# Performance work log

Measured on AMD Instinct MI355X. Metric: run time of the kernel, lower is better.

Reference implementation:

```python
import jax, jax.numpy as jnp
import numpy as np

N_NODES = 100000
N_EDGES = 1600000
D_IN = 128
D_HID = 128


def gcn_layer(x, src, dst, ew, W, b, n):
    """PyG GCNConv with normalize=True, add_self_loops=True (self-loop weight 1)."""
    h = x @ W  # [n, d_out]
    # degree includes self-loop weight 1.0
    deg = jax.ops.segment_sum(ew, dst, num_segments=n) + 1.0  # [n]
    dis = jnp.where(deg > 0, jax.lax.rsqrt(deg), 0.0)  # deg^{-1/2}
    norm = dis[src] * ew * dis[dst]  # [E]
    agg = jax.ops.segment_sum(norm[:, None] * h[src], dst, num_segments=n)
    # self-loop term: norm_ii = dis[i] * 1.0 * dis[i]
    agg = agg + (dis * dis)[:, None] * h
    return agg + b


def prelu(x, alpha):
    return jnp.where(x >= 0, x, alpha * x)


def setup_inputs() -> dict:
    key = jax.random.key(0)
    ks = jax.random.split(key, 12)
    x = jax.random.normal(ks[0], (N_NODES, D_IN), dtype=jnp.float32)
    edge_index = jax.random.randint(ks[1], (2, N_EDGES), 0, N_NODES, dtype=jnp.int64)
    edge_weight = jax.random.uniform(ks[2], (N_EDGES,), dtype=jnp.float32)
    s1 = 1.0 / np.sqrt(D_IN)
    s2 = 1.0 / np.sqrt(D_HID)
    params = {
        "W1": jax.random.normal(ks[3], (D_IN, D_HID), dtype=jnp.float32) * s1,
        "b1": jnp.zeros((D_HID,), dtype=jnp.float32),
        "a1": jnp.full((D_HID,), 0.25, dtype=jnp.float32),
        "W2": jax.random.normal(ks[4], (D_HID, D_HID), dtype=jnp.float32) * s2,
        "b2": jnp.zeros((D_HID,), dtype=jnp.float32),
        "a2": jnp.full((D_HID,), 0.25, dtype=jnp.float32),
        "W3": jax.random.normal(ks[5], (D_HID, D_HID), dtype=jnp.float32) * s2,
        "b3": jnp.zeros((D_HID,), dtype=jnp.float32),
        "a3": jnp.full((D_HID,), 0.25, dtype=jnp.float32),
    }
    return {"x": x, "edge_index": edge_index, "edge_weight": edge_weight, **params}


def reference(x, edge_index, edge_weight, W1, b1, a1, W2, b2, a2, W3, b3, a3):
    src, dst = edge_index[0], edge_index[1]
    n = x.shape[0]
    h = prelu(gcn_layer(x, src, dst, edge_weight, W1, b1, n), a1)
    h = prelu(gcn_layer(h, src, dst, edge_weight, W2, b2, n), a2)
    h = prelu(gcn_layer(h, src, dst, edge_weight, W3, b3, n), a3)
    return h
```

## Files before the change

kernel.cpp:

```cpp
#include <hip/hip_runtime.h>

#define N_NODES 100000
#define N_EDGES 1600000
#define D 128
#define TILE_ROWS 32
#define CHUNK 4096
#define NC ((N_EDGES + CHUNK - 1) / CHUNK)
#define NB ((N_NODES + 255) / 256)
#define HLEN (NB * NC)
#define SCAN_BLK ((HLEN + 1023) / 1024)

typedef unsigned int uint;
typedef unsigned long long u64;
typedef short short8 __attribute__((ext_vector_type(8)));
typedef float f32x4 __attribute__((ext_vector_type(4)));

__device__ inline ushort f2bf(float f) {
    union { float f; uint u; } v; v.f = f;
    uint r = v.u + 0x7fffu + ((v.u >> 16) & 1u);
    return (ushort)(r >> 16);
}
__device__ inline float bf2f(ushort b) {
    union { uint u; float f; } v; v.u = ((uint)b) << 16;
    return v.f;
}


__global__ __launch_bounds__(256) void k_hist(const int* __restrict__ dst, int* __restrict__ H) {
    __shared__ int hist[NB];
    int c = blockIdx.x;
    for (int i = threadIdx.x; i < NB; i += 256) hist[i] = 0;
    __syncthreads();
    int base = c * CHUNK;
    int lim = N_EDGES - base; if (lim > CHUNK) lim = CHUNK;
    for (int k = threadIdx.x; k < lim; k += 256)
        atomicAdd(&hist[dst[base + k] >> 8], 1);
    __syncthreads();
    for (int i = threadIdx.x; i < NB; i += 256) H[c * NB + i] = hist[i];
}

__global__ __launch_bounds__(256) void k_scanA(const int* __restrict__ H, int* __restrict__ HOFF,
                                               int* __restrict__ bsum) {
    __shared__ int sd[256];
    int t = threadIdx.x;
    int base = blockIdx.x * 1024 + t * 4;
    int v[4];
#pragma unroll
    for (int j = 0; j < 4; ++j) {
        int l = base + j;
        v[j] = (l < HLEN) ? H[(l % NC) * NB + (l / NC)] : 0;
    }
    int lsum = v[0] + v[1] + v[2] + v[3];
    sd[t] = lsum;
    __syncthreads();
    for (int off = 1; off < 256; off <<= 1) {
        int x = (t >= off) ? sd[t - off] : 0;
        __syncthreads();
        sd[t] += x;
        __syncthreads();
    }
    int excl = sd[t] - lsum;
    if (base + 0 < HLEN) HOFF[base + 0] = excl;
    if (base + 1 < HLEN) HOFF[base + 1] = excl + v[0];
    if (base + 2 < HLEN) HOFF[base + 2] = excl + v[0] + v[1];
    if (base + 3 < HLEN) HOFF[base + 3] = excl + v[0] + v[1] + v[2];
    if (t == 255) bsum[blockIdx.x] = sd[255];
}

__global__ void k_scanB(int* __restrict__ bsum) {
    if (blockIdx.x == 0 && threadIdx.x == 0) {
        int total = 0;
        for (int b = 0; b < SCAN_BLK; ++b) { int x = bsum[b]; bsum[b] = total; total += x; }
    }
}

__global__ void k_scanC(int* __restrict__ HOFF, const int* __restrict__ bsum) {
    int i = blockIdx.x * blockDim.x + threadIdx.x;
    if (i < HLEN) HOFF[i] += bsum[i >> 10];
}

__global__ __launch_bounds__(256) void k_pscat(const int* __restrict__ src, const int* __restrict__ dst,
                                               const float* __restrict__ ew, const int* __restrict__ HOFF,
                                               u64* __restrict__ tmp) {
    __shared__ int cur[NB];
    int c = blockIdx.x;
    for (int i = threadIdx.x; i < NB; i += 256) cur[i] = HOFF[i * NC + c];
    __syncthreads();
    int base = c * CHUNK;
    int lim = N_EDGES - base; if (lim > CHUNK) lim = CHUNK;
    for (int k = threadIdx.x; k < lim; k += 256) {
        int e = base + k;
        int s = src[e], t = dst[e];
        u64 q = (u64)llrintf(ew[e] * 1073741824.0f);
        int pos = atomicAdd(&cur[t >> 8], 1);
        tmp[pos] = (u64)s | ((u64)t << 17) | (q << 34);
    }
}

__global__ __launch_bounds__(256) void k_b1(const int* __restrict__ HOFF, const u64* __restrict__ tmp,
                                            float* __restrict__ dis, int* __restrict__ rowptr) {
    __shared__ int cnt[256];
    __shared__ u64 degq[256];
    __shared__ int sd[256];
    __shared__ int sbeg, send;
    int b = blockIdx.x, t = threadIdx.x;
    cnt[t] = 0; degq[t] = 0;
    if (t == 0) {
        sbeg = HOFF[b * NC];
        send = (b + 1 < NB) ? HOFF[(b + 1) * NC] : N_EDGES;
    }
    __syncthreads();
    int beg = sbeg, end = send, lo = b << 8;
    for (int e = beg + t; e < end; e += 256) {
        u64 r = tmp[e];
        int loc = (int)((r >> 17) & 0x1FFFF) - lo;
        atomicAdd(&cnt[loc], 1);
        atomicAdd(&degq[loc], r >> 34);
    }
    __syncthreads();
    int n = lo + t;
    if (n < N_NODES) {
        float deg = (float)((double)degq[t] * (1.0 / 1073741824.0));
        dis[n] = rsqrtf(deg + 1.0f);
    }
    int v = cnt[t];
    sd[t] = v;
    __syncthreads();
    for (int off = 1; off < 256; off <<= 1) {
        int x = (t >= off) ? sd[t - off] : 0;
        __syncthreads();
        sd[t] += x;
        __syncthreads();
    }
    if (n < N_NODES) rowptr[n] = beg + sd[t] - v;
    if (b == NB - 1 && t == 0) rowptr[N_NODES] = N_EDGES;
}

__global__ __launch_bounds__(256) void k_b2(const int* __restrict__ HOFF, const u64* __restrict__ tmp,
                                            const float* __restrict__ dis, const int* __restrict__ rowptr,
                                            int2* __restrict__ edges) {
    __shared__ int cur[256];
    __shared__ float disl[256];
    __shared__ int sbeg, send;
    int b = blockIdx.x, t = threadIdx.x;
    int lo = b << 8;
    int n = lo + t;
    cur[t] = (n < N_NODES) ? rowptr[n] : 0;
    disl[t] = (n < N_NODES) ? dis[n] : 0.0f;
    if (t == 0) {
        sbeg = HOFF[b * NC];
        send = (b + 1 < NB) ? HOFF[(b + 1) * NC] : N_EDGES;
    }
    __syncthreads();
    for (int e = sbeg + t; e < send; e += 256) {
        u64 r = tmp[e];
        int s = (int)(r & 0x1FFFF);
        int loc = (int)((r >> 17) & 0x1FFFF) - lo;
        float w = (float)(r >> 34) * (1.0f / 1073741824.0f);
        float coef = dis[s] * w * disl[loc];
        int pos = atomicAdd(&cur[loc], 1);
        edges[pos] = make_int2(s, __float_as_int(coef));
    }
}

__global__ void k_wsplit(const float* __restrict__ W, ushort* __restrict__ Wht,
                         ushort* __restrict__ Wlt) {
    int i = blockIdx.x * 256 + threadIdx.x;
    int k = i >> 7, c = i & 127;
    float w = W[i];
    ushort wh = f2bf(w);
    ushort wl = f2bf(w - bf2f(wh));
    int j = k >> 3;
    int off = c * 128 + (((j ^ (c & 7)) << 3) | (k & 7));
    Wht[off] = wh;
    Wlt[off] = wl;
}

__global__ __launch_bounds__(256) void k_gemm_mfma(
    const float* __restrict__ x, const ushort* __restrict__ Wht,
    const ushort* __restrict__ Wlt, ushort* __restrict__ hb)
{
    __shared__ ushort WH[16384];
    __shared__ ushort WL[16384];
    __shared__ ushort XH[4096];
    __shared__ ushort XL[4096];

    const int tx = threadIdx.x;
    const int row0 = blockIdx.x * TILE_ROWS;

    for (int i = tx; i < 2048; i += 256) {
        ((uint4*)WH)[i] = ((const uint4*)Wht)[i];
        ((uint4*)WL)[i] = ((const uint4*)Wlt)[i];
    }

    {
        int m = tx * 2;
        int r = m >> 4;
        int jb = m & 15;
        const float* xp = x + (size_t)(row0 + r) * D;
#pragma unroll
        for (int c = 0; c < 2; ++c) {
            int j = jb + c;
            float4 a0 = *(const float4*)(xp + j * 8);
            float4 a1 = *(const float4*)(xp + j * 8 + 4);
            float v[8] = {a0.x, a0.y, a0.z, a0.w, a1.x, a1.y, a1.z, a1.w};
            uint4 uh, ul;
            uint* ph = (uint*)&uh; uint* pl = (uint*)&ul;
#pragma unroll
            for (int e = 0; e < 4; ++e) {
                ushort h0 = f2bf(v[2 * e]),     h1 = f2bf(v[2 * e + 1]);
                ushort l0 = f2bf(v[2 * e] - bf2f(h0));
                ushort l1 = f2bf(v[2 * e + 1] - bf2f(h1));
                ph[e] = (uint)h0 | ((uint)h1 << 16);
                pl[e] = (uint)l0 | ((uint)l1 << 16);
            }
            int off = r * 16 + (j ^ (r & 7));
            ((uint4*)XH)[off] = uh;
            ((uint4*)XL)[off] = ul;
        }
    }
    __syncthreads();

    const int wv = tx >> 6;
    const int lane = tx & 63;
    const int lr = lane & 15;
    const int g = lane >> 4;

    f32x4 acc[2][2] = {};

    const int c0 = wv * 32 + lr;
    const int c1 = c0 + 16;

#pragma unroll
    for (int ks = 0; ks < 4; ++ks) {
        int co = ((ks * 4 + g) ^ (lr & 7)) << 3;
        short8 ah0 = *(short8*)&XH[lr * 128 + co];
        short8 ah1 = *(short8*)&XH[(16 + lr) * 128 + co];
        short8 al0 = *(short8*)&XL[lr * 128 + co];
        short8 al1 = *(short8*)&XL[(16 + lr) * 128 + co];
        short8 bh0 = *(short8*)&WH[c0 * 128 + co];
        short8 bh1 = *(short8*)&WH[c1 * 128 + co];
        short8 bl0 = *(short8*)&WL[c0 * 128 + co];
        short8 bl1 = *(short8*)&WL[c1 * 128 + co];

        acc[0][0] = __builtin_amdgcn_mfma_f32_16x16x32_bf16(ah0, bh0, acc[0][0], 0, 0, 0);
        acc[0][1] = __builtin_amdgcn_mfma_f32_16x16x32_bf16(ah0, bh1, acc[0][1], 0, 0, 0);
        acc[1][0] = __builtin_amdgcn_mfma_f32_16x16x32_bf16(ah1, bh0, acc[1][0], 0, 0, 0);
        acc[1][1] = __builtin_amdgcn_mfma_f32_16x16x32_bf16(ah1, bh1, acc[1][1], 0, 0, 0);
        acc[0][0] = __builtin_amdgcn_mfma_f32_16x16x32_bf16(al0, bh0, acc[0][0], 0, 0, 0);
        acc[0][1] = __builtin_amdgcn_mfma_f32_16x16x32_bf16(al0, bh1, acc[0][1], 0, 0, 0);
        acc[1][0] = __builtin_amdgcn_mfma_f32_16x16x32_bf16(al1, bh0, acc[1][0], 0, 0, 0);
        acc[1][1] = __builtin_amdgcn_mfma_f32_16x16x32_bf16(al1, bh1, acc[1][1], 0, 0, 0);
        acc[0][0] = __builtin_amdgcn_mfma_f32_16x16x32_bf16(ah0, bl0, acc[0][0], 0, 0, 0);
        acc[0][1] = __builtin_amdgcn_mfma_f32_16x16x32_bf16(ah0, bl1, acc[0][1], 0, 0, 0);
        acc[1][0] = __builtin_amdgcn_mfma_f32_16x16x32_bf16(ah1, bl0, acc[1][0], 0, 0, 0);
        acc[1][1] = __builtin_amdgcn_mfma_f32_16x16x32_bf16(ah1, bl1, acc[1][1], 0, 0, 0);
    }

#pragma unroll
    for (int rt = 0; rt < 2; ++rt) {
#pragma unroll
        for (int ct = 0; ct < 2; ++ct) {
            int colb = wv * 32 + ct * 16 + lr;
#pragma unroll
            for (int e = 0; e < 4; ++e) {
                int row = row0 + rt * 16 + g * 4 + e;
                hb[(size_t)row * D + colb] = f2bf(acc[rt][ct][e]);
            }
        }
    }
}

__global__ __launch_bounds__(256) void k_gather(
    const int* __restrict__ rowptr, const int2* __restrict__ edges,
    const ushort* __restrict__ hb, const float* __restrict__ dis,
    const float* __restrict__ b, const float* __restrict__ alpha,
    float* __restrict__ out)
{
    int gid = blockIdx.x * 256 + threadIdx.x;
    int n = gid >> 6;
    if (n >= N_NODES) return;
    int lane = gid & 63;
    int q = lane >> 4;
    int c0 = (lane & 15) * 8;

    int beg = rowptr[n], end = rowptr[n + 1];
    float acc[8] = {0.f, 0.f, 0.f, 0.f, 0.f, 0.f, 0.f, 0.f};

    int e = beg + q;
    for (; e + 12 < end; e += 16) {
        int2 sc0 = edges[e];
        int2 sc1 = edges[e + 4];
        int2 sc2 = edges[e + 8];
        int2 sc3 = edges[e + 12];
        uint4 hv0 = *(const uint4*)&hb[(size_t)sc0.x * D + c0];
        uint4 hv1 = *(const uint4*)&hb[(size_t)sc1.x * D + c0];
        uint4 hv2 = *(const uint4*)&hb[(size_t)sc2.x * D + c0];
        uint4 hv3 = *(const uint4*)&hb[(size_t)sc3.x * D + c0];
        float ca = __int_as_float(sc0.y);
        float cb = __int_as_float(sc1.y);
        float cc = __int_as_float(sc2.y);
        float cd = __int_as_float(sc3.y);
#pragma unroll
        for (int j = 0; j < 4; ++j) {
            uint w0 = ((const uint*)&hv0)[j];
            uint w1 = ((const uint*)&hv1)[j];
            uint w2 = ((const uint*)&hv2)[j];
            uint w3 = ((const uint*)&hv3)[j];
            acc[2 * j]     = fmaf(ca, __uint_as_float(w0 << 16),         acc[2 * j]);
            acc[2 * j + 1] = fmaf(ca, __uint_as_float(w0 & 0xffff0000u), acc[2 * j + 1]);
            acc[2 * j]     = fmaf(cb, __uint_as_float(w1 << 16),         acc[2 * j]);
            acc[2 * j + 1] = fmaf(cb, __uint_as_float(w1 & 0xffff0000u), acc[2 * j + 1]);
            acc[2 * j]     = fmaf(cc, __uint_as_float(w2 << 16),         acc[2 * j]);
            acc[2 * j + 1] = fmaf(cc, __uint_as_float(w2 & 0xffff0000u), acc[2 * j + 1]);
            acc[2 * j]     = fmaf(cd, __uint_as_float(w3 << 16),         acc[2 * j]);
            acc[2 * j + 1] = fmaf(cd, __uint_as_float(w3 & 0xffff0000u), acc[2 * j + 1]);
        }
    }
    for (; e < end; e += 4) {
        int2 sc = edges[e];
        float c = __int_as_float(sc.y);
        uint4 hv = *(const uint4*)&hb[(size_t)sc.x * D + c0];
#pragma unroll
        for (int j = 0; j < 4; ++j) {
            uint w = ((const uint*)&hv)[j];
            acc[2 * j]     = fmaf(c, __uint_as_float(w << 16),         acc[2 * j]);
            acc[2 * j + 1] = fmaf(c, __uint_as_float(w & 0xffff0000u), acc[2 * j + 1]);
        }
    }

#pragma unroll
    for (int j = 0; j < 8; ++j) {
        acc[j] += __shfl_xor(acc[j], 16);
        acc[j] += __shfl_xor(acc[j], 32);
    }

    if (q == 0) {
        float di = dis[n];
        float d2 = di * di;
        uint4 hv = *(const uint4*)&hb[(size_t)n * D + c0];
        float r[8];
#pragma unroll
        for (int j = 0; j < 4; ++j) {
            uint w = ((const uint*)&hv)[j];
            float lo = __uint_as_float(w << 16);
            float hi = __uint_as_float(w & 0xffff0000u);
            r[2 * j]     = acc[2 * j]     + d2 * lo + b[c0 + 2 * j];
            r[2 * j + 1] = acc[2 * j + 1] + d2 * hi + b[c0 + 2 * j + 1];
        }
#pragma unroll
        for (int j = 0; j < 8; ++j) {
            float av = alpha[c0 + j];
            r[j] = r[j] >= 0.f ? r[j] : av * r[j];
        }
        *(float4*)&out[(size_t)n * D + c0]     = make_float4(r[0], r[1], r[2], r[3]);
        *(float4*)&out[(size_t)n * D + c0 + 4] = make_float4(r[4], r[5], r[6], r[7]);
    }
}


extern "C" void kernel_launch(void* const* d_in, const int* in_sizes, int n_in,
                              void* d_out, int out_size, void* d_ws, size_t ws_size,
                              hipStream_t stream) {
    const float* x   = (const float*)d_in[0];
    const int*   ei  = (const int*)d_in[1];
    const float* ew  = (const float*)d_in[2];
    const float* W1  = (const float*)d_in[3];
    const float* b1  = (const float*)d_in[4];
    const float* a1  = (const float*)d_in[5];
    const float* W2  = (const float*)d_in[6];
    const float* b2  = (const float*)d_in[7];
    const float* a2  = (const float*)d_in[8];
    const float* W3  = (const float*)d_in[9];
    const float* b3  = (const float*)d_in[10];
    const float* a3  = (const float*)d_in[11];

    const int* src = ei;
    const int* dst = ei + N_EDGES;

    float* out = (float*)d_out;

    ushort* hb    = (ushort*)d_ws;
    int2*   edges = (int2*)(hb + (size_t)N_NODES * D);
    u64*    tmp   = (u64*)(edges + N_EDGES);
    int*    H     = (int*)(tmp + N_EDGES);
    int*    HOFF  = H + HLEN;
    int*    bsum  = HOFF + HLEN;
    float*  dis   = (float*)(bsum + 256);
    int*    rowptr= (int*)(dis + N_NODES);
    ushort* wsp   = (ushort*)(rowptr + N_NODES + 2);
    ushort* Wht1 = wsp;              ushort* Wlt1 = wsp + 16384;
    ushort* Wht2 = wsp + 2 * 16384;  ushort* Wlt2 = wsp + 3 * 16384;
    ushort* Wht3 = wsp + 4 * 16384;  ushort* Wlt3 = wsp + 5 * 16384;

    k_wsplit<<<64, 256, 0, stream>>>(W1, Wht1, Wlt1);
    k_wsplit<<<64, 256, 0, stream>>>(W2, Wht2, Wlt2);
    k_wsplit<<<64, 256, 0, stream>>>(W3, Wht3, Wlt3);

    k_hist<<<NC, 256, 0, stream>>>(dst, H);
    k_scanA<<<SCAN_BLK, 256, 0, stream>>>(H, HOFF, bsum);
    k_scanB<<<1, 1, 0, stream>>>(bsum);
    k_scanC<<<(HLEN + 255) / 256, 256, 0, stream>>>(HOFF, bsum);
    k_pscat<<<NC, 256, 0, stream>>>(src, dst, ew, HOFF, tmp);
    k_b1<<<NB, 256, 0, stream>>>(HOFF, tmp, dis, rowptr);
    k_b2<<<NB, 256, 0, stream>>>(HOFF, tmp, dis, rowptr, edges);

    const int gemm_blocks   = N_NODES / TILE_ROWS;
    const int gather_blocks = (N_NODES * 64) / 256;

    k_gemm_mfma<<<gemm_blocks, 256, 0, stream>>>(x, Wht1, Wlt1, hb);
    k_gather<<<gather_blocks, 256, 0, stream>>>(rowptr, edges, hb, dis, b1, a1, out);
    k_gemm_mfma<<<gemm_blocks, 256, 0, stream>>>(out, Wht2, Wlt2, hb);
    k_gather<<<gather_blocks, 256, 0, stream>>>(rowptr, edges, hb, dis, b2, a2, out);
    k_gemm_mfma<<<gemm_blocks, 256, 0, stream>>>(out, Wht3, Wlt3, hb);
    k_gather<<<gather_blocks, 256, 0, stream>>>(rowptr, edges, hb, dis, b3, a3, out);
}
```

Baseline: 415.9 us.

## Persistent GEMM blocks, parallel block-sum scan, merged weight split, shallower gather unroll

The GEMM becomes a grid-stride persistent kernel with 512 blocks, so the 64 KB bf16 hi/lo weight tile is loaded into shared memory once per block rather than once per 32-row tile. The single-thread block-sum scan is replaced by a 256-thread shared-memory scan, and the three weight-split launches are merged into one. The gather inner loop is unrolled by 2 instead of 4 edges, which lowers register pressure and may raise occupancy but leaves fewer independent loads in flight. The persistent GEMM adds an extra barrier per tile and only 512 blocks may underfill the device.

After: 384.3 us. 1.08x faster.

```diff
diff --git a/kernel.cpp b/kernel.cpp
--- a/kernel.cpp
+++ b/kernel.cpp
@@ -4,6 +4,8 @@
 #define N_EDGES 1600000
 #define D 128
 #define TILE_ROWS 32
+#define N_TILES (N_NODES / TILE_ROWS)
+#define GEMM_BLOCKS 512
 #define CHUNK 4096
 #define NC ((N_EDGES + CHUNK - 1) / CHUNK)
 #define NB ((N_NODES + 255) / 256)
@@ -67,11 +69,19 @@
     if (t == 255) bsum[blockIdx.x] = sd[255];
 }
 
-__global__ void k_scanB(int* __restrict__ bsum) {
-    if (blockIdx.x == 0 && threadIdx.x == 0) {
-        int total = 0;
-        for (int b = 0; b < SCAN_BLK; ++b) { int x = bsum[b]; bsum[b] = total; total += x; }
-    }
+__global__ __launch_bounds__(256) void k_scanB(int* __restrict__ bsum) {
+    __shared__ int sd[256];
+    int t = threadIdx.x;
+    int v = (t < SCAN_BLK) ? bsum[t] : 0;
+    sd[t] = v;
+    __syncthreads();
+    for (int off = 1; off < 256; off <<= 1) {
+        int x = (t >= off) ? sd[t - off] : 0;
+        __syncthreads();
+        sd[t] += x;
+        __syncthreads();
+    }
+    if (t < SCAN_BLK) bsum[t] = sd[t] - v;
 }
 
 __global__ void k_scanC(int* __restrict__ HOFF, const int* __restrict__ bsum) {
@@ -163,9 +173,14 @@
     }
 }
 
-__global__ void k_wsplit(const float* __restrict__ W, ushort* __restrict__ Wht,
-                         ushort* __restrict__ Wlt) {
-    int i = blockIdx.x * 256 + threadIdx.x;
+__global__ void k_wsplit3(const float* __restrict__ W1, const float* __restrict__ W2,
+                          const float* __restrict__ W3, ushort* __restrict__ wsp) {
+    int gid = blockIdx.x * 256 + threadIdx.x;
+    int l = gid >> 14;
+    int i = gid & 16383;
+    const float* W = (l == 0) ? W1 : (l == 1) ? W2 : W3;
+    ushort* Wht = wsp + l * 32768;
+    ushort* Wlt = Wht + 16384;
     int k = i >> 7, c = i & 127;
     float w = W[i];
     ushort wh = f2bf(w);
@@ -186,86 +201,88 @@
     __shared__ ushort XL[4096];
 
     const int tx = threadIdx.x;
-    const int row0 = blockIdx.x * TILE_ROWS;
 
     for (int i = tx; i < 2048; i += 256) {
         ((uint4*)WH)[i] = ((const uint4*)Wht)[i];
         ((uint4*)WL)[i] = ((const uint4*)Wlt)[i];
     }
-
-    {
-        int m = tx * 2;
-        int r = m >> 4;
-        int jb = m & 15;
-        const float* xp = x + (size_t)(row0 + r) * D;
-#pragma unroll
-        for (int c = 0; c < 2; ++c) {
-            int j = jb + c;
-            float4 a0 = *(const float4*)(xp + j * 8);
-            float4 a1 = *(const float4*)(xp + j * 8 + 4);
-            float v[8] = {a0.x, a0.y, a0.z, a0.w, a1.x, a1.y, a1.z, a1.w};
-            uint4 uh, ul;
-            uint* ph = (uint*)&uh; uint* pl = (uint*)&ul;
-#pragma unroll
-            for (int e = 0; e < 4; ++e) {
-                ushort h0 = f2bf(v[2 * e]),     h1 = f2bf(v[2 * e + 1]);
-                ushort l0 = f2bf(v[2 * e] - bf2f(h0));
-                ushort l1 = f2bf(v[2 * e + 1] - bf2f(h1));
-                ph[e] = (uint)h0 | ((uint)h1 << 16);
-                pl[e] = (uint)l0 | ((uint)l1 << 16);
-            }
-            int off = r * 16 + (j ^ (r & 7));
-            ((uint4*)XH)[off] = uh;
-            ((uint4*)XL)[off] = ul;
-        }
-    }
-    __syncthreads();
 
     const int wv = tx >> 6;
     const int lane = tx & 63;
     const int lr = lane & 15;
     const int g = lane >> 4;
-
-    f32x4 acc[2][2] = {};
-
     const int c0 = wv * 32 + lr;
     const int c1 = c0 + 16;
 
-#pragma unroll
-    for (int ks = 0; ks < 4; ++ks) {
-        int co = ((ks * 4 + g) ^ (lr & 7)) << 3;
-        short8 ah0 = *(short8*)&XH[lr * 128 + co];
-        short8 ah1 = *(short8*)&XH[(16 + lr) * 128 + co];
-        short8 al0 = *(short8*)&XL[lr * 128 + co];
-        short8 al1 = *(short8*)&XL[(16 + lr) * 128 + co];
-        short8 bh0 = *(short8*)&WH[c0 * 128 + co];
-        short8 bh1 = *(short8*)&WH[c1 * 128 + co];
-        short8 bl0 = *(short8*)&WL[c0 * 128 + co];
-        short8 bl1 = *(short8*)&WL[c1 * 128 + co];
-
-        acc[0][0] = __builtin_amdgcn_mfma_f32_16x16x32_bf16(ah0, bh0, acc[0][0], 0, 0, 0);
-        acc[0][1] = __builtin_amdgcn_mfma_f32_16x16x32_bf16(ah0, bh1, acc[0][1], 0, 0, 0);
-        acc[1][0] = __builtin_amdgcn_mfma_f32_16x16x32_bf16(ah1, bh0, acc[1][0], 0, 0, 0);
-        acc[1][1] = __builtin_amdgcn_mfma_f32_16x16x32_bf16(ah1, bh1, acc[1][1], 0, 0, 0);
-        acc[0][0] = __builtin_amdgcn_mfma_f32_16x16x32_bf16(al0, bh0, acc[0][0], 0, 0, 0);
-        acc[0][1] = __builtin_amdgcn_mfma_f32_16x16x32_bf16(al0, bh1, acc[0][1], 0, 0, 0);
-        acc[1][0] = __builtin_amdgcn_mfma_f32_16x16x32_bf16(al1, bh0, acc[1][0], 0, 0, 0);
-        acc[1][1] = __builtin_amdgcn_mfma_f32_16x16x32_bf16(al1, bh1, acc[1][1], 0, 0, 0);
-        acc[0][0] = __builtin_amdgcn_mfma_f32_16x16x32_bf16(ah0, bl0, acc[0][0], 0, 0, 0);
-        acc[0][1] = __builtin_amdgcn_mfma_f32_16x16x32_bf16(ah0, bl1, acc[0][1], 0, 0, 0);
-        acc[1][0] = __builtin_amdgcn_mfma_f32_16x16x32_bf16(ah1, bl0, acc[1][0], 0, 0, 0);
-        acc[1][1] = __builtin_amdgcn_mfma_f32_16x16x32_bf16(ah1, bl1, acc[1][1], 0, 0, 0);
-    }
-
-#pragma unroll
-    for (int rt = 0; rt < 2; ++rt) {
-#pragma unroll
-        for (int ct = 0; ct < 2; ++ct) {
-            int colb = wv * 32 + ct * 16 + lr;
-#pragma unroll
-            for (int e = 0; e < 4; ++e) {
-                int row = row0 + rt * 16 + g * 4 + e;
-                hb[(size_t)row * D + colb] = f2bf(acc[rt][ct][e]);
+    const int xr = (tx * 2) >> 4;
+    const int xjb = (tx * 2) & 15;
+
+    for (int tile = blockIdx.x; tile < N_TILES; tile += GEMM_BLOCKS) {
+        const int row0 = tile * TILE_ROWS;
+        __syncthreads();
+
+        {
+            const float* xp = x + (size_t)(row0 + xr) * D;
+#pragma unroll
+            for (int c = 0; c < 2; ++c) {
+                int j = xjb + c;
+                float4 a0 = *(const float4*)(xp + j * 8);
+                float4 a1 = *(const float4*)(xp + j * 8 + 4);
+                float v[8] = {a0.x, a0.y, a0.z, a0.w, a1.x, a1.y, a1.z, a1.w};
+                uint4 uh, ul;
+                uint* ph = (uint*)&uh; uint* pl = (uint*)&ul;
+#pragma unroll
+                for (int e = 0; e < 4; ++e) {
+                    ushort h0 = f2bf(v[2 * e]),     h1 = f2bf(v[2 * e + 1]);
+                    ushort l0 = f2bf(v[2 * e] - bf2f(h0));
+                    ushort l1 = f2bf(v[2 * e + 1] - bf2f(h1));
+                    ph[e] = (uint)h0 | ((uint)h1 << 16);
+                    pl[e] = (uint)l0 | ((uint)l1 << 16);
+                }
+                int off = xr * 16 + (j ^ (xr & 7));
+                ((uint4*)XH)[off] = uh;
+                ((uint4*)XL)[off] = ul;
+            }
+        }
+        __syncthreads();
+
+        f32x4 acc[2][2] = {};
+#pragma unroll
+        for (int ks = 0; ks < 4; ++ks) {
+            int co = ((ks * 4 + g) ^ (lr & 7)) << 3;
+            short8 ah0 = *(short8*)&XH[lr * 128 + co];
+            short8 ah1 = *(short8*)&XH[(16 + lr) * 128 + co];
+            short8 al0 = *(short8*)&XL[lr * 128 + co];
+            short8 al1 = *(short8*)&XL[(16 + lr) * 128 + co];
+            short8 bh0 = *(short8*)&WH[c0 * 128 + co];
+            short8 bh1 = *(short8*)&WH[c1 * 128 + co];
+            short8 bl0 = *(short8*)&WL[c0 * 128 + co];
+            short8 bl1 = *(short8*)&WL[c1 * 128 + co];
+
+            acc[0][0] = __builtin_amdgcn_mfma_f32_16x16x32_bf16(ah0, bh0, acc[0][0], 0, 0, 0);
+            acc[0][1] = __builtin_amdgcn_mfma_f32_16x16x32_bf16(ah0, bh1, acc[0][1], 0, 0, 0);
+            acc[1][0] = __builtin_amdgcn_mfma_f32_16x16x32_bf16(ah1, bh0, acc[1][0], 0, 0, 0);
+            acc[1][1] = __builtin_amdgcn_mfma_f32_16x16x32_bf16(ah1, bh1, acc[1][1], 0, 0, 0);
+            acc[0][0] = __builtin_amdgcn_mfma_f32_16x16x32_bf16(al0, bh0, acc[0][0], 0, 0, 0);
+            acc[0][1] = __builtin_amdgcn_mfma_f32_16x16x32_bf16(al0, bh1, acc[0][1], 0, 0, 0);
+            acc[1][0] = __builtin_amdgcn_mfma_f32_16x16x32_bf16(al1, bh0, acc[1][0], 0, 0, 0);
+            acc[1][1] = __builtin_amdgcn_mfma_f32_16x16x32_bf16(al1, bh1, acc[1][1], 0, 0, 0);
+            acc[0][0] = __builtin_amdgcn_mfma_f32_16x16x32_bf16(ah0, bl0, acc[0][0], 0, 0, 0);
+            acc[0][1] = __builtin_amdgcn_mfma_f32_16x16x32_bf16(ah0, bl1, acc[0][1], 0, 0, 0);
+            acc[1][0] = __builtin_amdgcn_mfma_f32_16x16x32_bf16(ah1, bl0, acc[1][0], 0, 0, 0);
+            acc[1][1] = __builtin_amdgcn_mfma_f32_16x16x32_bf16(ah1, bl1, acc[1][1], 0, 0, 0);
+        }
+
+#pragma unroll
+        for (int rt = 0; rt < 2; ++rt) {
+#pragma unroll
+            for (int ct = 0; ct < 2; ++ct) {
+                int colb = wv * 32 + ct * 16 + lr;
+#pragma unroll
+                for (int e = 0; e < 4; ++e) {
+                    int row = row0 + rt * 16 + g * 4 + e;
+                    hb[(size_t)row * D + colb] = f2bf(acc[rt][ct][e]);
+                }
             }
         }
     }
@@ -288,36 +305,24 @@
     float acc[8] = {0.f, 0.f, 0.f, 0.f, 0.f, 0.f, 0.f, 0.f};
 
     int e = beg + q;
-    for (; e + 12 < end; e += 16) {
+    for (; e + 4 < end; e += 8) {
         int2 sc0 = edges[e];
         int2 sc1 = edges[e + 4];
-        int2 sc2 = edges[e + 8];
-        int2 sc3 = edges[e + 12];
         uint4 hv0 = *(const uint4*)&hb[(size_t)sc0.x * D + c0];
         uint4 hv1 = *(const uint4*)&hb[(size_t)sc1.x * D + c0];
-        uint4 hv2 = *(const uint4*)&hb[(size_t)sc2.x * D + c0];
-        uint4 hv3 = *(const uint4*)&hb[(size_t)sc3.x * D + c0];
         float ca = __int_as_float(sc0.y);
         float cb = __int_as_float(sc1.y);
-        float cc = __int_as_float(sc2.y);
-        float cd = __int_as_float(sc3.y);
 #pragma unroll
         for (int j = 0; j < 4; ++j) {
             uint w0 = ((const uint*)&hv0)[j];
             uint w1 = ((const uint*)&hv1)[j];
-            uint w2 = ((const uint*)&hv2)[j];
-            uint w3 = ((const uint*)&hv3)[j];
             acc[2 * j]     = fmaf(ca, __uint_as_float(w0 << 16),         acc[2 * j]);
             acc[2 * j + 1] = fmaf(ca, __uint_as_float(w0 & 0xffff0000u), acc[2 * j + 1]);
             acc[2 * j]     = fmaf(cb, __uint_as_float(w1 << 16),         acc[2 * j]);
             acc[2 * j + 1] = fmaf(cb, __uint_as_float(w1 & 0xffff0000u), acc[2 * j + 1]);
-            acc[2 * j]     = fmaf(cc, __uint_as_float(w2 << 16),         acc[2 * j]);
-            acc[2 * j + 1] = fmaf(cc, __uint_as_float(w2 & 0xffff0000u), acc[2 * j + 1]);
-            acc[2 * j]     = fmaf(cd, __uint_as_float(w3 << 16),         acc[2 * j]);
-            acc[2 * j + 1] = fmaf(cd, __uint_as_float(w3 & 0xffff0000u), acc[2 * j + 1]);
-        }
-    }
-    for (; e < end; e += 4) {
+        }
+    }
+    if (e < end) {
         int2 sc = edges[e];
         float c = __int_as_float(sc.y);
         uint4 hv = *(const uint4*)&hb[(size_t)sc.x * D + c0];
@@ -389,29 +394,26 @@
     float*  dis   = (float*)(bsum + 256);
     int*    rowptr= (int*)(dis + N_NODES);
     ushort* wsp   = (ushort*)(rowptr + N_NODES + 2);
-    ushort* Wht1 = wsp;              ushort* Wlt1 = wsp + 16384;
-    ushort* Wht2 = wsp + 2 * 16384;  ushort* Wlt2 = wsp + 3 * 16384;
-    ushort* Wht3 = wsp + 4 * 16384;  ushort* Wlt3 = wsp + 5 * 16384;
-
-    k_wsplit<<<64, 256, 0, stream>>>(W1, Wht1, Wlt1);
-    k_wsplit<<<64, 256, 0, stream>>>(W2, Wht2, Wlt2);
-    k_wsplit<<<64, 256, 0, stream>>>(W3, Wht3, Wlt3);
+    ushort* Wht1 = wsp;             ushort* Wlt1 = wsp + 16384;
+    ushort* Wht2 = wsp + 32768;     ushort* Wlt2 = wsp + 32768 + 16384;
+    ushort* Wht3 = wsp + 65536;     ushort* Wlt3 = wsp + 65536 + 16384;
+
+    k_wsplit3<<<192, 256, 0, stream>>>(W1, W2, W3, wsp);
 
     k_hist<<<NC, 256, 0, stream>>>(dst, H);
     k_scanA<<<SCAN_BLK, 256, 0, stream>>>(H, HOFF, bsum);
-    k_scanB<<<1, 1, 0, stream>>>(bsum);
+    k_scanB<<<1, 256, 0, stream>>>(bsum);
     k_scanC<<<(HLEN + 255) / 256, 256, 0, stream>>>(HOFF, bsum);
     k_pscat<<<NC, 256, 0, stream>>>(src, dst, ew, HOFF, tmp);
     k_b1<<<NB, 256, 0, stream>>>(HOFF, tmp, dis, rowptr);
     k_b2<<<NB, 256, 0, stream>>>(HOFF, tmp, dis, rowptr, edges);
 
-    const int gemm_blocks   = N_NODES / TILE_ROWS;
     const int gather_blocks = (N_NODES * 64) / 256;
 
-    k_gemm_mfma<<<gemm_blocks, 256, 0, stream>>>(x, Wht1, Wlt1, hb);
+    k_gemm_mfma<<<GEMM_BLOCKS, 256, 0, stream>>>(x, Wht1, Wlt1, hb);
     k_gather<<<gather_blocks, 256, 0, stream>>>(rowptr, edges, hb, dis, b1, a1, out);
-    k_gemm_mfma<<<gemm_blocks, 256, 0, stream>>>(out, Wht2, Wlt2, hb);
+    k_gemm_mfma<<<GEMM_BLOCKS, 256, 0, stream>>>(out, Wht2, Wlt2, hb);
     k_gather<<<gather_blocks, 256, 0, stream>>>(rowptr, edges, hb, dis, b2, a2, out);
-    k_gemm_mfma<<<gemm_blocks, 256, 0, stream>>>(out, Wht3, Wlt3, hb);
+    k_gemm_mfma<<<GEMM_BLOCKS, 256, 0, stream>>>(out, Wht3, Wlt3, hb);
     k_gather<<<gather_blocks, 256, 0, stream>>>(rowptr, edges, hb, dis, b3, a3, out);
 }
```
